# Optimization experiments

Hardware: AMD Instinct MI355X
Metric: run time of the kernel (lower is better)

Reference implementation:

```python
import jax, jax.numpy as jnp
import numpy as np

N, E, G = 32768, 262144, 512
IN_DIM, HID, HEADS = 300, 128, 4
D_FUSED = HID * HEADS  # 512
L = 3


def setup_inputs() -> dict:
    key = jax.random.key(0)
    ks = jax.random.split(key, 24)
    s = 0.02
    inp = {
        "x": jax.random.normal(ks[0], (N, IN_DIM), jnp.float32),
        "edge_index": jax.random.randint(ks[1], (2, E), 0, N, jnp.int32),
        "batch": jnp.sort(jax.random.randint(ks[2], (N,), 0, G, jnp.int32)),
        "syn_w": jax.random.normal(ks[3], (IN_DIM, HID)) * s,
        "syn_b": jnp.zeros((HID,), jnp.float32),
        "ant_w": jax.random.normal(ks[4], (IN_DIM, HID)) * s,
        "ant_b": jnp.zeros((HID,), jnp.float32),
        "fusion_w": jax.random.normal(ks[5], (2 * HID, D_FUSED)) * s,
        "fusion_b": jnp.zeros((D_FUSED,), jnp.float32),
        "Wq": jax.random.normal(ks[6], (L, D_FUSED, D_FUSED)) * s,
        "bq": jnp.zeros((L, D_FUSED), jnp.float32),
        "Wk": jax.random.normal(ks[7], (L, D_FUSED, D_FUSED)) * s,
        "bk": jnp.zeros((L, D_FUSED), jnp.float32),
        "Wv": jax.random.normal(ks[8], (L, D_FUSED, D_FUSED)) * s,
        "bv": jnp.zeros((L, D_FUSED), jnp.float32),
        "Wskip": jax.random.normal(ks[9], (L, D_FUSED, D_FUSED)) * s,
        "bskip": jnp.zeros((L, D_FUSED), jnp.float32),
        "cls_w1": jax.random.normal(ks[10], (D_FUSED, HID)) * s,
        "cls_b1": jnp.zeros((HID,), jnp.float32),
        "cls_w2": jax.random.normal(ks[11], (HID, 1)) * s,
        "cls_b2": jnp.zeros((1,), jnp.float32),
    }
    return inp


def _transformer_conv(h, src, dst, Wq, bq, Wk, bk, Wv, bv, Wskip, bskip):
    # PyG TransformerConv: per-edge dot-product attention, softmax over in-neighbors of dst,
    # concat heads, plus root/skip linear (root_weight=True, concat=True, no edge_attr).
    n = h.shape[0]
    q = (h @ Wq + bq).reshape(n, HEADS, HID)
    k = (h @ Wk + bk).reshape(n, HEADS, HID)
    v = (h @ Wv + bv).reshape(n, HEADS, HID)
    scale = 1.0 / np.sqrt(HID)
    logits = jnp.einsum("ehd,ehd->eh", q[dst], k[src]) * scale  # [E, H]
    m = jax.ops.segment_max(logits, dst, num_segments=n)        # [N, H]
    e = jnp.exp(logits - m[dst])
    z = jax.ops.segment_sum(e, dst, num_segments=n)
    alpha = e / (z[dst] + 1e-16)                                # [E, H]
    msg = alpha[:, :, None] * v[src]                            # [E, H, D]
    out = jax.ops.segment_sum(msg, dst, num_segments=n).reshape(n, D_FUSED)
    return out + h @ Wskip + bskip


def reference(x, edge_index, batch, syn_w, syn_b, ant_w, ant_b, fusion_w, fusion_b,
              Wq, bq, Wk, bk, Wv, bv, Wskip, bskip, cls_w1, cls_b1, cls_w2, cls_b2):
    x_syn = jax.nn.relu(x @ syn_w + syn_b)
    x_ant = jax.nn.relu(x @ ant_w + ant_b)
    h = jnp.concatenate([x_syn, x_ant], axis=1) @ fusion_w + fusion_b  # [N, 512]
    src, dst = edge_index[0], edge_index[1]
    for l in range(L):
        h = jax.nn.relu(_transformer_conv(h, src, dst, Wq[l], bq[l], Wk[l], bk[l],
                                          Wv[l], bv[l], Wskip[l], bskip[l]))
    cnt = jax.ops.segment_sum(jnp.ones((h.shape[0],), h.dtype), batch, num_segments=G)
    pooled = jax.ops.segment_sum(h, batch, num_segments=G) / jnp.maximum(cnt, 1.0)[:, None]
    hid = jax.nn.relu(pooled @ cls_w1 + cls_b1)
    out = jax.nn.sigmoid(hid @ cls_w2 + cls_b2)
    return out.squeeze()
```

## Files before the change

kernel.cpp:

```cpp
#include <hip/hip_runtime.h>
#include <hip/hip_bf16.h>
#include <hip/hip_fp8.h>
#include <math.h>

#define N_NODES 32768
#define N_EDGES 262144
#define N_GRAPHS 512
#define IN_DIM 300
#define KPAD 320
#define HID 128
#define HEADS 4
#define D_FUSED 512
#define N_LAYERS 3

typedef __hip_bfloat16 bf16;
typedef short bf16x8 __attribute__((ext_vector_type(8)));
typedef float f32x4 __attribute__((ext_vector_type(4)));
typedef float f32x2 __attribute__((ext_vector_type(2)));

__device__ __forceinline__ float bfs_to_f(short s)
{
    unsigned u = ((unsigned)(unsigned short)s) << 16;
    return __builtin_bit_cast(float, u);
}

__device__ __forceinline__ short f_to_bfs(float v)
{
    return (short)__builtin_bit_cast(unsigned short, __float2bfloat16(v));
}

__device__ __forceinline__ void bf8_to_f32(bf16x8 v, float* f)
{
#pragma unroll
    for (int j = 0; j < 8; ++j) f[j] = bfs_to_f(v[j]);
}

__device__ __forceinline__ unsigned char f32_to_fp8(float v)
{
#if __has_builtin(__builtin_amdgcn_cvt_pk_fp8_f32)
    int p = __builtin_amdgcn_cvt_pk_fp8_f32(v, v, 0, false);
    return (unsigned char)(p & 0xff);
#else
    __hip_fp8_e4m3 t(v);
    return (unsigned char)t.__x;
#endif
}

__device__ __forceinline__ void fp8x8_to_f32(uint2 w, float* f)
{
#if __has_builtin(__builtin_amdgcn_cvt_pk_f32_fp8)
    f32x2 a = __builtin_amdgcn_cvt_pk_f32_fp8((int)w.x, false);
    f32x2 b = __builtin_amdgcn_cvt_pk_f32_fp8((int)w.x, true);
    f32x2 c = __builtin_amdgcn_cvt_pk_f32_fp8((int)w.y, false);
    f32x2 d = __builtin_amdgcn_cvt_pk_f32_fp8((int)w.y, true);
    f[0] = a.x; f[1] = a.y; f[2] = b.x; f[3] = b.y;
    f[4] = c.x; f[5] = c.y; f[6] = d.x; f[7] = d.y;
#else
    const unsigned char* p = (const unsigned char*)&w;
#pragma unroll
    for (int j = 0; j < 8; ++j) {
        __hip_fp8_e4m3 t;
        t.__x = (__hip_fp8_storage_t)p[j];
        f[j] = (float)t;
    }
#endif
}

__device__ __forceinline__ void gload_lds16(const void* g, void* l)
{
    __builtin_amdgcn_global_load_lds(
        (const __attribute__((address_space(1))) void*)g,
        (__attribute__((address_space(3))) void*)l, 16, 0, 0);
}

template <int K, int ACT, int EPI>
__global__ __launch_bounds__(512, 2) void mfma_gemm256(
    const bf16* __restrict__ A, int lda,
    const bf16* __restrict__ Bt,
    const float* __restrict__ bias,
    bf16* __restrict__ C0, int ldc0,
    bf16* __restrict__ C1, int ldc1, int csplit,
    unsigned char* __restrict__ C2,
    int nbx)
{
    __shared__ __align__(16) char lds[131072];

    const int t = threadIdx.x;
    const int wid = t >> 6, lane = t & 63;
    const int hi = lane >> 4, li = lane & 15;
    const int wr = wid >> 2, wc = wid & 3;

    int wg = blockIdx.x;
    if ((gridDim.x & 7) == 0) {
        const int cpx = gridDim.x >> 3;
        wg = (wg & 7) * cpx + (wg >> 3);
    }
    const int mb = wg / nbx, nb = wg % nbx;
    const int brow = mb * 256, bcol = nb * 256;
    constexpr int NT = K >> 6;

    const int row0 = t >> 3, sl0 = (((t & 7) ^ (row0 & 7)) * 8);
    const int c1i = t + 512;
    const int row1 = c1i >> 3, sl1 = (((c1i & 7) ^ (row1 & 7)) * 8);

    const bf16* srcs[4][2];
    srcs[0][0] = A  + (size_t)(brow + row0)       * lda + sl0;
    srcs[0][1] = A  + (size_t)(brow + row1)       * lda + sl1;
    srcs[1][0] = A  + (size_t)(brow + 128 + row0) * lda + sl0;
    srcs[1][1] = A  + (size_t)(brow + 128 + row1) * lda + sl1;
    srcs[2][0] = Bt + (size_t)(bcol + row0)       * K   + sl0;
    srcs[2][1] = Bt + (size_t)(bcol + row1)       * K   + sl1;
    srcs[3][0] = Bt + (size_t)(bcol + 128 + row0) * K   + sl0;
    srcs[3][1] = Bt + (size_t)(bcol + 128 + row1) * K   + sl1;

    auto stage_part = [&](int buf, int kt1, int q) {
        const int ko = kt1 * 64;
        const int slab = buf * 65536 + (q >> 1) * 32768 + (q & 1) * 16384;
        gload_lds16(srcs[q][0] + ko, lds + slab + wid * 1024);
        gload_lds16(srcs[q][1] + ko, lds + slab + 8192 + wid * 1024);
    };

    f32x4 acc[8][4] = {};

#pragma unroll
    for (int q = 0; q < 4; ++q) stage_part(0, 0, q);

#pragma unroll
    for (int kt = 0; kt < NT; ++kt) {
        const int b = kt & 1;
        const char* Aslab = lds + b * 65536 + wr * 16384;
        const char* Bslab = lds + b * 65536 + 32768 + (wc >> 1) * 16384;
        const int bRow0 = (wc & 1) * 64;

        if (kt < NT - 1) {
            stage_part(b ^ 1, kt + 1, 0);
            asm volatile("s_waitcnt vmcnt(2)" ::: "memory");
        } else {
            asm volatile("s_waitcnt vmcnt(0)" ::: "memory");
        }
        __builtin_amdgcn_s_barrier();
        __builtin_amdgcn_sched_barrier(0);

        bf16x8 bfrag[4][2];
#pragma unroll
        for (int q = 0; q < 4; ++q) {
            if (q > 0 && kt < NT - 1) stage_part(b ^ 1, kt + 1, q);
            if (q == 0) {
#pragma unroll
                for (int n = 0; n < 4; ++n)
#pragma unroll
                    for (int ks = 0; ks < 2; ++ks) {
                        const int row = bRow0 + n * 16 + li;
                        bfrag[n][ks] = *(const bf16x8*)(
                            Bslab + row * 128 + (((ks * 4 + hi) ^ (row & 7)) << 4));
                    }
            }
            bf16x8 af[2][2];
#pragma unroll
            for (int mm = 0; mm < 2; ++mm)
#pragma unroll
                for (int ks = 0; ks < 2; ++ks) {
                    const int row = (q * 2 + mm) * 16 + li;
                    af[mm][ks] = *(const bf16x8*)(
                        Aslab + row * 128 + (((ks * 4 + hi) ^ (row & 7)) << 4));
                }
            __builtin_amdgcn_s_barrier();
            __builtin_amdgcn_s_setprio(1);
#pragma unroll
            for (int ks = 0; ks < 2; ++ks)
#pragma unroll
                for (int mm = 0; mm < 2; ++mm)
#pragma unroll
                    for (int n = 0; n < 4; ++n)
                        acc[q * 2 + mm][n] = __builtin_amdgcn_mfma_f32_16x16x32_bf16(
                            af[mm][ks], bfrag[n][ks], acc[q * 2 + mm][n], 0, 0, 0);
            __builtin_amdgcn_s_setprio(0);
            __builtin_amdgcn_s_barrier();
        }
    }

    if (EPI == 0) {
        const bool lo = (bcol < csplit);
        bf16* Cd = lo ? C0 : C1;
        const int ldc = lo ? ldc0 : ldc1;
        const int csub = lo ? 0 : csplit;
#pragma unroll
        for (int m = 0; m < 8; ++m)
#pragma unroll
            for (int n = 0; n < 4; ++n) {
                const int col = bcol + wc * 64 + n * 16 + li;
                const float bv = bias[col];
#pragma unroll
                for (int r = 0; r < 4; ++r) {
                    const int row = brow + wr * 128 + m * 16 + hi * 4 + r;
                    float v = acc[m][n][r] + bv;
                    if (ACT == 1) v = fmaxf(v, 0.f);
                    Cd[(size_t)row * ldc + (col - csub)] = __float2bfloat16(v);
                }
            }
    } else if (bcol < 512) {
#pragma unroll
        for (int m = 0; m < 8; ++m)
#pragma unroll
            for (int n = 0; n < 4; ++n) {
                const int col = bcol + wc * 64 + n * 16 + li;
                const float bv = bias[col];
#pragma unroll
                for (int r = 0; r < 4; ++r) {
                    const int row = brow + wr * 128 + m * 16 + hi * 4 + r;
                    C0[(size_t)row * ldc0 + col] = __float2bfloat16(acc[m][n][r] + bv);
                }
            }
    } else if (bcol < 1024) {
#pragma unroll
        for (int m = 0; m < 8; ++m)
#pragma unroll
            for (int n = 0; n < 4; ++n) {
                const int col = bcol + wc * 64 + n * 16 + li;
                const float bv = bias[col];
#pragma unroll
                for (int r = 0; r < 4; ++r) {
                    const int row = brow + wr * 128 + m * 16 + hi * 4 + r;
                    C1[(size_t)row * ldc1 + (col - 512)] = __float2bfloat16(acc[m][n][r] + bv);
                }
            }
    } else {
#pragma unroll
        for (int m = 0; m < 8; ++m)
#pragma unroll
            for (int n = 0; n < 4; ++n) {
                const int col = bcol + wc * 64 + n * 16 + li;
                const float bv = bias[col];
#pragma unroll
                for (int r = 0; r < 4; ++r) {
                    const int row = brow + wr * 128 + m * 16 + hi * 4 + r;
                    C2[(size_t)row * 1024 + (col - 1024)] = f32_to_fp8(acc[m][n][r] + bv);
                }
            }
    }
}

template <int ACT>
__global__ __launch_bounds__(256) void mfma_gemm(
    const bf16* __restrict__ A, int lda,
    const bf16* __restrict__ Bt,
    const float* __restrict__ bias,
    bf16* __restrict__ C, int ldc, int K)
{
    __shared__ __align__(16) char lds[16384];
    char* As = lds;
    char* Bs = lds + 8192;

    const int t = threadIdx.x;
    const int wid = t >> 6, lane = t & 63;
    const int brow = blockIdx.x * 128;
    const int bcol = blockIdx.y * 128;
    const int wr = wid >> 1, wc = wid & 1;

    f32x4 acc[4][4] = {};

    for (int k0 = 0; k0 < K; k0 += 32) {
#pragma unroll
        for (int j = 0; j < 2; ++j) {
            const int seg = wid * 2 + j;
            const int row = seg * 16 + (lane >> 2);
            const int clin = lane & 3;
            const int clog = clin ^ ((row >> 1) & 3);
            gload_lds16(A + (size_t)(brow + row) * lda + k0 + clog * 8,
                        As + seg * 1024);
            gload_lds16(Bt + (size_t)(bcol + row) * K + k0 + clog * 8,
                        Bs + seg * 1024);
        }
        __syncthreads();

        bf16x8 af[4], bfr[4];
#pragma unroll
        for (int m = 0; m < 4; ++m) {
            const int row = wr * 64 + m * 16 + (lane & 15);
            const int cl = (lane >> 4) ^ ((row >> 1) & 3);
            af[m] = *(const bf16x8*)(As + row * 64 + cl * 16);
        }
#pragma unroll
        for (int n = 0; n < 4; ++n) {
            const int row = wc * 64 + n * 16 + (lane & 15);
            const int cl = (lane >> 4) ^ ((row >> 1) & 3);
            bfr[n] = *(const bf16x8*)(Bs + row * 64 + cl * 16);
        }
#pragma unroll
        for (int m = 0; m < 4; ++m)
#pragma unroll
            for (int n = 0; n < 4; ++n)
                acc[m][n] = __builtin_amdgcn_mfma_f32_16x16x32_bf16(
                    af[m], bfr[n], acc[m][n], 0, 0, 0);
        __syncthreads();
    }

#pragma unroll
    for (int m = 0; m < 4; ++m) {
#pragma unroll
        for (int n = 0; n < 4; ++n) {
            const int col = bcol + wc * 64 + n * 16 + (lane & 15);
            const float bv = bias[col];
#pragma unroll
            for (int r = 0; r < 4; ++r) {
                const int row = brow + wr * 64 + m * 16 + (lane >> 4) * 4 + r;
                float v = acc[m][n][r] + bv;
                if (ACT == 1) v = fmaxf(v, 0.f);
                C[(size_t)row * ldc + col] = __float2bfloat16(v);
            }
        }
    }
}

__global__ void prep_xpad_kernel(const float* __restrict__ x, bf16* __restrict__ xb)
{
    const int n = blockIdx.x, k = threadIdx.x;
    xb[(size_t)n * KPAD + k] =
        __float2bfloat16(k < IN_DIM ? x[(size_t)n * IN_DIM + k] : 0.f);
}

__global__ void prep_encw_kernel(const float* __restrict__ syn_w,
                                 const float* __restrict__ ant_w,
                                 bf16* __restrict__ wt)
{
    const int c = blockIdx.x, k = threadIdx.x;
    float v = 0.f;
    if (k < IN_DIM) v = (c < HID) ? syn_w[k * HID + c] : ant_w[k * HID + (c - HID)];
    wt[c * KPAD + k] = __float2bfloat16(v);
}

__global__ void prep_fusw_kernel(const float* __restrict__ fw, bf16* __restrict__ wt)
{
    const int c = blockIdx.x, k = threadIdx.x;
    wt[c * 256 + k] = __float2bfloat16(fw[k * D_FUSED + c]);
}

__global__ __launch_bounds__(256) void prep_combw_kernel(
    const float* __restrict__ Wskip,
    const float* __restrict__ Wq,
    const float* __restrict__ Wk,
    const float* __restrict__ Wv,
    bf16* __restrict__ wt)
{
    __shared__ float tile[32][33];
    const int blk = blockIdx.x;
    const int l = blk >> 10, rem = blk & 1023;
    const int cb = rem >> 4, kb = rem & 15;
    const int c0 = cb * 32;

    const int sel = c0 >> 9;
    const float* mat = (sel == 0) ? Wskip : (sel == 1) ? Wq : (sel == 2) ? Wk : Wv;
    const int cp0 = c0 & 511;

    const int j = threadIdx.x & 31;
    const int i0 = threadIdx.x >> 5;
#pragma unroll
    for (int s = 0; s < 4; ++s) {
        const int i = i0 + 8 * s;
        tile[i][j] = mat[((size_t)l * 512 + kb * 32 + i) * 512 + cp0 + j];
    }
    __syncthreads();
#pragma unroll
    for (int s = 0; s < 4; ++s) {
        const int jj = i0 + 8 * s;
        wt[((size_t)l * 2048 + c0 + jj) * 512 + kb * 32 + j] =
            __float2bfloat16(tile[j][jj]);
    }
}

__global__ void prep_bias_kernel(const float* __restrict__ syn_b,
                                 const float* __restrict__ ant_b,
                                 const float* __restrict__ bskip,
                                 const float* __restrict__ bq,
                                 const float* __restrict__ bk,
                                 const float* __restrict__ bv,
                                 float* __restrict__ benc,
                                 float* __restrict__ bcomb)
{
    const int i = blockIdx.x * 256 + threadIdx.x;
    if (i < 256) benc[i] = (i < HID) ? syn_b[i] : ant_b[i - HID];
    const int j = i - 256;
    if (j >= 0 && j < 6144) {
        const int l = j >> 11, c = j & 2047;
        const int sel = c >> 9, col = c & 511;
        const float* s = (sel == 0) ? bskip : (sel == 1) ? bq : (sel == 2) ? bk : bv;
        bcomb[j] = s[l * D_FUSED + col];
    }
}

__global__ void zero_int_kernel(int* __restrict__ p, int n)
{
    int i = blockIdx.x * 256 + threadIdx.x;
    if (i < n) p[i] = 0;
}

__global__ void hist_kernel(const int* __restrict__ dst, int* __restrict__ deg, int E)
{
    int e = blockIdx.x * 256 + threadIdx.x;
    if (e < E) atomicAdd(&deg[dst[e]], 1);
}

__global__ __launch_bounds__(256) void partial_sum_kernel(const int* __restrict__ deg,
                                                          int* __restrict__ part)
{
    int v = deg[blockIdx.x * 256 + threadIdx.x];
#pragma unroll
    for (int o = 32; o; o >>= 1) v += __shfl_xor(v, o);
    __shared__ int w4[4];
    if ((threadIdx.x & 63) == 0) w4[threadIdx.x >> 6] = v;
    __syncthreads();
    if (threadIdx.x == 0) part[blockIdx.x] = w4[0] + w4[1] + w4[2] + w4[3];
}

__global__ __launch_bounds__(128) void scan_part_kernel(int* __restrict__ part)
{
    __shared__ int s[128];
    const int t = threadIdx.x;
    s[t] = part[t];
    __syncthreads();
    for (int o = 1; o < 128; o <<= 1) {
        int v = (t >= o) ? s[t - o] : 0;
        __syncthreads();
        s[t] += v;
        __syncthreads();
    }
    part[t] = (t == 0) ? 0 : s[t - 1];
}

__global__ __launch_bounds__(256) void off_kernel(const int* __restrict__ deg,
                                                  const int* __restrict__ part,
                                                  int* __restrict__ off)
{
    __shared__ int s[256];
    const int b = blockIdx.x, t = threadIdx.x;
    s[t] = deg[b * 256 + t];
    __syncthreads();
    for (int o = 1; o < 256; o <<= 1) {
        int v = (t >= o) ? s[t - o] : 0;
        __syncthreads();
        s[t] += v;
        __syncthreads();
    }
    const int excl = (t == 0) ? 0 : s[t - 1];
    off[b * 256 + t] = part[b] + excl;
    if (b == 127 && t == 255) off[N_NODES] = part[127] + s[255];
}

__global__ void scatter_kernel(const int* __restrict__ src, const int* __restrict__ dst,
                               const int* __restrict__ off, int* __restrict__ cursor,
                               int* __restrict__ csr_src, int E)
{
    int e = blockIdx.x * 256 + threadIdx.x;
    if (e < E) {
        int d = dst[e];
        int pos = atomicAdd(&cursor[d], 1);
        csr_src[off[d] + pos] = src[e];
    }
}

__global__ __launch_bounds__(256) void attn_kernel(
    const bf16* __restrict__ qb, const unsigned char* __restrict__ kvb,
    bf16* __restrict__ hout, const int* __restrict__ off,
    const int* __restrict__ csr)
{
    const int n = blockIdx.x;
    const int hd = threadIdx.x >> 6;
    const int lane = threadIdx.x & 63;
    const int g = lane >> 4, sub = lane & 15;
    const float scale = 0.08838834764831845f;

    float qf[8];
    bf8_to_f32(*(const bf16x8*)(qb + (size_t)n * 512 + hd * 128 + sub * 8), qf);

    float zA = 0.f, zB = 0.f;
    float accA[8] = {}, accB[8] = {};

    const int s0 = off[n], s1 = off[n + 1];
    for (int e0 = s0; e0 < s1; e0 += 8) {
        const int ea = e0 + g;
        const int eb = e0 + 4 + g;
        const bool va = (ea < s1);
        const bool vb = (eb < s1);
        const int sa = va ? csr[ea] : 0;
        const int sb = vb ? csr[eb] : 0;
        const unsigned char* kpa = kvb + (size_t)sa * 1024 + hd * 128 + sub * 8;
        const unsigned char* kpb = kvb + (size_t)sb * 1024 + hd * 128 + sub * 8;

        const uint2 kwa = *(const uint2*)kpa;
        const uint2 kwb = *(const uint2*)kpb;
        const uint2 vwa = *(const uint2*)(kpa + 512);
        const uint2 vwb = *(const uint2*)(kpb + 512);

        float kfa[8], kfb[8];
        fp8x8_to_f32(kwa, kfa);
        fp8x8_to_f32(kwb, kfb);
        float da = 0.f, db = 0.f;
#pragma unroll
        for (int j = 0; j < 8; ++j) {
            da = fmaf(qf[j], kfa[j], da);
            db = fmaf(qf[j], kfb[j], db);
        }
        da += __shfl_xor(da, 1);  db += __shfl_xor(db, 1);
        da += __shfl_xor(da, 2);  db += __shfl_xor(db, 2);
        da += __shfl_xor(da, 4);  db += __shfl_xor(db, 4);
        da += __shfl_xor(da, 8);  db += __shfl_xor(db, 8);

        const float wa = va ? __expf(da * scale) : 0.f;
        const float wb = vb ? __expf(db * scale) : 0.f;
        zA += wa;
        zB += wb;

        float vfa[8], vfb[8];
        fp8x8_to_f32(vwa, vfa);
        fp8x8_to_f32(vwb, vfb);
#pragma unroll
        for (int j = 0; j < 8; ++j) {
            accA[j] = fmaf(wa, vfa[j], accA[j]);
            accB[j] = fmaf(wb, vfb[j], accB[j]);
        }
    }

    float zz = zA + zB;
    zz += __shfl_xor(zz, 16);
    zz += __shfl_xor(zz, 32);
    const float inv = 1.f / (zz + 1e-16f);

    float o[8];
#pragma unroll
    for (int j = 0; j < 8; ++j) {
        float a = accA[j] + accB[j];
        a += __shfl_xor(a, 16);
        a += __shfl_xor(a, 32);
        o[j] = a * inv;
    }

    if (g == 0) {
        const size_t ob = (size_t)n * D_FUSED + hd * HID + sub * 8;
        const bf16x8 sk = *(const bf16x8*)(hout + ob);
        bf16x8 res;
#pragma unroll
        for (int j = 0; j < 8; ++j)
            res[j] = f_to_bfs(fmaxf(o[j] + bfs_to_f(sk[j]), 0.f));
        *(bf16x8*)(hout + ob) = res;
    }
}

__global__ __launch_bounds__(256) void pool_kernel(const bf16* __restrict__ h,
                                                   const int* __restrict__ batch,
                                                   float* __restrict__ pooled)
{
    const int g = blockIdx.x;
    int a = 0, b = N_NODES;
    while (a < b) { int mid = (a + b) >> 1; if (batch[mid] < g) a = mid + 1; else b = mid; }
    const int start = a;
    b = N_NODES;
    while (a < b) { int mid = (a + b) >> 1; if (batch[mid] < g + 1) a = mid + 1; else b = mid; }
    const int end = a;
    const float invc = 1.f / fmaxf((float)(end - start), 1.f);

    const int t = threadIdx.x;
    float2 s = make_float2(0.f, 0.f);
    for (int nidx = start; nidx < end; ++nidx) {
        const bf16* p = h + (size_t)nidx * D_FUSED + t * 2;
        s.x += bfs_to_f(((const short*)p)[0]);
        s.y += bfs_to_f(((const short*)p)[1]);
    }
    pooled[(size_t)g * D_FUSED + t * 2]     = s.x * invc;
    pooled[(size_t)g * D_FUSED + t * 2 + 1] = s.y * invc;
}

__global__ __launch_bounds__(128) void cls_kernel(const float* __restrict__ pooled,
                                                  const float* __restrict__ w1,
                                                  const float* __restrict__ b1,
                                                  const float* __restrict__ w2,
                                                  const float* __restrict__ b2,
                                                  float* __restrict__ out)
{
    const int g = blockIdx.x;
    const int j = threadIdx.x;
    const float* p = pooled + (size_t)g * D_FUSED;
    float acc = 0.f;
    for (int i = 0; i < D_FUSED; ++i) acc += p[i] * w1[i * HID + j];
    const float hid = fmaxf(acc + b1[j], 0.f);
    float val = hid * w2[j];
#pragma unroll
    for (int o = 32; o; o >>= 1) val += __shfl_xor(val, o);
    __shared__ float ws2[2];
    if ((threadIdx.x & 63) == 0) ws2[threadIdx.x >> 6] = val;
    __syncthreads();
    if (threadIdx.x == 0) {
        const float sum = ws2[0] + ws2[1] + b2[0];
        out[g] = 1.f / (1.f + __expf(-sum));
    }
}

extern "C" void kernel_launch(void* const* d_in, const int* in_sizes, int n_in,
                              void* d_out, int out_size, void* d_ws, size_t ws_size,
                              hipStream_t stream)
{
    const float* x        = (const float*)d_in[0];
    const int*   ei       = (const int*)d_in[1];
    const int*   batch    = (const int*)d_in[2];
    const float* syn_w    = (const float*)d_in[3];
    const float* syn_b    = (const float*)d_in[4];
    const float* ant_w    = (const float*)d_in[5];
    const float* ant_b    = (const float*)d_in[6];
    const float* fusion_w = (const float*)d_in[7];
    const float* fusion_b = (const float*)d_in[8];
    const float* Wq       = (const float*)d_in[9];
    const float* bq       = (const float*)d_in[10];
    const float* Wk       = (const float*)d_in[11];
    const float* bk       = (const float*)d_in[12];
    const float* Wv       = (const float*)d_in[13];
    const float* bv       = (const float*)d_in[14];
    const float* Wskip    = (const float*)d_in[15];
    const float* bskip    = (const float*)d_in[16];
    const float* cls_w1   = (const float*)d_in[17];
    const float* cls_b1   = (const float*)d_in[18];
    const float* cls_w2   = (const float*)d_in[19];
    const float* cls_b2   = (const float*)d_in[20];

    const int* src = ei;
    const int* dst = ei + N_EDGES;

    const size_t NV = (size_t)N_NODES * D_FUSED;
    bf16* hA    = (bf16*)d_ws;
    bf16* hB    = hA + NV;
    bf16* qbuf  = hB + NV;
    unsigned char* kvbuf = (unsigned char*)(qbuf + NV);
    bf16* wenc  = (bf16*)(kvbuf + (size_t)N_NODES * 1024);
    bf16* wfus  = wenc + 256 * KPAD;
    bf16* wcomb = wfus + 512 * 256;
    float* benc = (float*)(wcomb + (size_t)3 * 2048 * 512);
    float* bcomb = benc + 256;
    float* pooled = bcomb + 6144;
    int* deg    = (int*)(pooled + (size_t)N_GRAPHS * D_FUSED);
    int* cursor = deg + N_NODES;
    int* part   = cursor + N_NODES;
    int* off    = part + 128;
    int* csr    = off + N_NODES + 1;

    bf16* xb   = qbuf;
    bf16* tenc = hB;

    zero_int_kernel<<<(2 * N_NODES + 255) / 256, 256, 0, stream>>>(deg, 2 * N_NODES);
    hist_kernel<<<N_EDGES / 256, 256, 0, stream>>>(dst, deg, N_EDGES);
    partial_sum_kernel<<<128, 256, 0, stream>>>(deg, part);
    scan_part_kernel<<<1, 128, 0, stream>>>(part);
    off_kernel<<<128, 256, 0, stream>>>(deg, part, off);
    scatter_kernel<<<N_EDGES / 256, 256, 0, stream>>>(src, dst, off, cursor, csr, N_EDGES);

    prep_xpad_kernel<<<N_NODES, KPAD, 0, stream>>>(x, xb);
    prep_encw_kernel<<<256, KPAD, 0, stream>>>(syn_w, ant_w, wenc);
    prep_fusw_kernel<<<512, 256, 0, stream>>>(fusion_w, wfus);
    prep_combw_kernel<<<3072, 256, 0, stream>>>(Wskip, Wq, Wk, Wv, wcomb);
    prep_bias_kernel<<<25, 256, 0, stream>>>(syn_b, ant_b, bskip, bq, bk, bv, benc, bcomb);

    mfma_gemm<1><<<dim3(N_NODES / 128, 2), 256, 0, stream>>>(
        xb, KPAD, wenc, benc, tenc, 256, KPAD);
    mfma_gemm256<256, 0, 0><<<256, 512, 0, stream>>>(
        tenc, 256, wfus, fusion_b, hA, D_FUSED, hA, D_FUSED, D_FUSED, nullptr, 2);

    bf16* hcur = hA;
    bf16* hnew = hB;
    for (int l = 0; l < N_LAYERS; ++l) {
        mfma_gemm256<512, 0, 1><<<1024, 512, 0, stream>>>(
            hcur, D_FUSED, wcomb + (size_t)l * 2048 * D_FUSED,
            bcomb + (size_t)l * 2048,
            hnew, D_FUSED, qbuf, D_FUSED, 512, kvbuf, 8);
        attn_kernel<<<N_NODES, 256, 0, stream>>>(qbuf, kvbuf, hnew, off, csr);
        bf16* tmp = hcur; hcur = hnew; hnew = tmp;
    }

    pool_kernel<<<N_GRAPHS, 256, 0, stream>>>(hcur, batch, pooled);
    cls_kernel<<<N_GRAPHS, 128, 0, stream>>>(pooled, cls_w1, cls_b1, cls_w2, cls_b2,
                                             (float*)d_out);
}
```

Baseline: 582.9 us.

## Store Q in fp8 alongside K/V, vectorize x padding and pooling

The GEMM epilogue now writes Q as fp8 into one interleaved 1536-byte-per-node QKV buffer instead of a separate bf16 Q buffer, and the attention kernel reads Q, K and V from that single buffer. This halves Q write and read traffic and drops one epilogue branch, at the cost of extra quantization error on Q. Separately, the x padding kernel moves from one element per thread to float4 loads with bf16x4 stores. The pooling kernel reads 8 bf16 values per thread across four node lanes and combines them with a shared-memory reduction.

Result: faster. 563.8 us (-3.3%).

```diff
diff --git a/kernel.cpp b/kernel.cpp
--- a/kernel.cpp
+++ b/kernel.cpp
@@ -15,6 +15,7 @@
 
 typedef __hip_bfloat16 bf16;
 typedef short bf16x8 __attribute__((ext_vector_type(8)));
+typedef short bf16x4 __attribute__((ext_vector_type(4)));
 typedef float f32x4 __attribute__((ext_vector_type(4)));
 typedef float f32x2 __attribute__((ext_vector_type(2)));
 
@@ -211,7 +212,7 @@
                     C0[(size_t)row * ldc0 + col] = __float2bfloat16(acc[m][n][r] + bv);
                 }
             }
-    } else if (bcol < 1024) {
+    } else {
 #pragma unroll
         for (int m = 0; m < 8; ++m)
 #pragma unroll
@@ -221,20 +222,7 @@
 #pragma unroll
                 for (int r = 0; r < 4; ++r) {
                     const int row = brow + wr * 128 + m * 16 + hi * 4 + r;
-                    C1[(size_t)row * ldc1 + (col - 512)] = __float2bfloat16(acc[m][n][r] + bv);
-                }
-            }
-    } else {
-#pragma unroll
-        for (int m = 0; m < 8; ++m)
-#pragma unroll
-            for (int n = 0; n < 4; ++n) {
-                const int col = bcol + wc * 64 + n * 16 + li;
-                const float bv = bias[col];
-#pragma unroll
-                for (int r = 0; r < 4; ++r) {
-                    const int row = brow + wr * 128 + m * 16 + hi * 4 + r;
-                    C2[(size_t)row * 1024 + (col - 1024)] = f32_to_fp8(acc[m][n][r] + bv);
+                    C2[(size_t)row * 1536 + (col - 512)] = f32_to_fp8(acc[m][n][r] + bv);
                 }
             }
     }
@@ -314,9 +302,17 @@
 
 __global__ void prep_xpad_kernel(const float* __restrict__ x, bf16* __restrict__ xb)
 {
-    const int n = blockIdx.x, k = threadIdx.x;
-    xb[(size_t)n * KPAD + k] =
-        __float2bfloat16(k < IN_DIM ? x[(size_t)n * IN_DIM + k] : 0.f);
+    const int idx = blockIdx.x * 256 + threadIdx.x;
+    const int n = idx / 80, q = idx % 80;
+    bf16x4 o;
+    if (q < 75) {
+        const float4 v = *(const float4*)(x + (size_t)n * IN_DIM + q * 4);
+        o[0] = f_to_bfs(v.x); o[1] = f_to_bfs(v.y);
+        o[2] = f_to_bfs(v.z); o[3] = f_to_bfs(v.w);
+    } else {
+        o[0] = 0; o[1] = 0; o[2] = 0; o[3] = 0;
+    }
+    *(bf16x4*)(xb + (size_t)n * KPAD + q * 4) = o;
 }
 
 __global__ void prep_encw_kernel(const float* __restrict__ syn_w,
@@ -459,9 +455,8 @@
 }
 
 __global__ __launch_bounds__(256) void attn_kernel(
-    const bf16* __restrict__ qb, const unsigned char* __restrict__ kvb,
-    bf16* __restrict__ hout, const int* __restrict__ off,
-    const int* __restrict__ csr)
+    const unsigned char* __restrict__ qkvb, bf16* __restrict__ hout,
+    const int* __restrict__ off, const int* __restrict__ csr)
 {
     const int n = blockIdx.x;
     const int hd = threadIdx.x >> 6;
@@ -470,7 +465,7 @@
     const float scale = 0.08838834764831845f;
 
     float qf[8];
-    bf8_to_f32(*(const bf16x8*)(qb + (size_t)n * 512 + hd * 128 + sub * 8), qf);
+    fp8x8_to_f32(*(const uint2*)(qkvb + (size_t)n * 1536 + hd * 128 + sub * 8), qf);
 
     float zA = 0.f, zB = 0.f;
     float accA[8] = {}, accB[8] = {};
@@ -483,13 +478,13 @@
         const bool vb = (eb < s1);
         const int sa = va ? csr[ea] : 0;
         const int sb = vb ? csr[eb] : 0;
-        const unsigned char* kpa = kvb + (size_t)sa * 1024 + hd * 128 + sub * 8;
-        const unsigned char* kpb = kvb + (size_t)sb * 1024 + hd * 128 + sub * 8;
-
-        const uint2 kwa = *(const uint2*)kpa;
-        const uint2 kwb = *(const uint2*)kpb;
-        const uint2 vwa = *(const uint2*)(kpa + 512);
-        const uint2 vwb = *(const uint2*)(kpb + 512);
+        const unsigned char* pa = qkvb + (size_t)sa * 1536 + hd * 128 + sub * 8;
+        const unsigned char* pb = qkvb + (size_t)sb * 1536 + hd * 128 + sub * 8;
+
+        const uint2 kwa = *(const uint2*)(pa + 512);
+        const uint2 kwb = *(const uint2*)(pb + 512);
+        const uint2 vwa = *(const uint2*)(pa + 1024);
+        const uint2 vwb = *(const uint2*)(pb + 1024);
 
         float kfa[8], kfb[8];
         fp8x8_to_f32(kwa, kfa);
@@ -558,15 +553,28 @@
     const int end = a;
     const float invc = 1.f / fmaxf((float)(end - start), 1.f);
 
-    const int t = threadIdx.x;
-    float2 s = make_float2(0.f, 0.f);
-    for (int nidx = start; nidx < end; ++nidx) {
-        const bf16* p = h + (size_t)nidx * D_FUSED + t * 2;
-        s.x += bfs_to_f(((const short*)p)[0]);
-        s.y += bfs_to_f(((const short*)p)[1]);
-    }
-    pooled[(size_t)g * D_FUSED + t * 2]     = s.x * invc;
-    pooled[(size_t)g * D_FUSED + t * 2 + 1] = s.y * invc;
+    const int nl = threadIdx.x >> 6;
+    const int dl = threadIdx.x & 63;
+
+    float s[8] = {};
+    for (int nidx = start + nl; nidx < end; nidx += 4) {
+        const bf16x8 v = *(const bf16x8*)(h + (size_t)nidx * D_FUSED + dl * 8);
+#pragma unroll
+        for (int j = 0; j < 8; ++j) s[j] += bfs_to_f(v[j]);
+    }
+
+    __shared__ float red[4][512];
+#pragma unroll
+    for (int j = 0; j < 8; ++j) red[nl][dl * 8 + j] = s[j];
+    __syncthreads();
+    if (nl == 0) {
+#pragma unroll
+        for (int j = 0; j < 8; ++j) {
+            const int d = dl * 8 + j;
+            pooled[(size_t)g * D_FUSED + d] =
+                (red[0][d] + red[1][d] + red[2][d] + red[3][d]) * invc;
+        }
+    }
 }
 
 __global__ __launch_bounds__(128) void cls_kernel(const float* __restrict__ pooled,
@@ -626,9 +634,8 @@
     const size_t NV = (size_t)N_NODES * D_FUSED;
     bf16* hA    = (bf16*)d_ws;
     bf16* hB    = hA + NV;
-    bf16* qbuf  = hB + NV;
-    unsigned char* kvbuf = (unsigned char*)(qbuf + NV);
-    bf16* wenc  = (bf16*)(kvbuf + (size_t)N_NODES * 1024);
+    unsigned char* qkv = (unsigned char*)(hB + NV);
+    bf16* wenc  = (bf16*)(qkv + (size_t)N_NODES * 1536);
     bf16* wfus  = wenc + 256 * KPAD;
     bf16* wcomb = wfus + 512 * 256;
     float* benc = (float*)(wcomb + (size_t)3 * 2048 * 512);
@@ -640,7 +647,7 @@
     int* off    = part + 128;
     int* csr    = off + N_NODES + 1;
 
-    bf16* xb   = qbuf;
+    bf16* xb   = (bf16*)qkv;
     bf16* tenc = hB;
 
     zero_int_kernel<<<(2 * N_NODES + 255) / 256, 256, 0, stream>>>(deg, 2 * N_NODES);
@@ -650,7 +657,7 @@
     off_kernel<<<128, 256, 0, stream>>>(deg, part, off);
     scatter_kernel<<<N_EDGES / 256, 256, 0, stream>>>(src, dst, off, cursor, csr, N_EDGES);
 
-    prep_xpad_kernel<<<N_NODES, KPAD, 0, stream>>>(x, xb);
+    prep_xpad_kernel<<<(N_NODES * 80) / 256, 256, 0, stream>>>(x, xb);
     prep_encw_kernel<<<256, KPAD, 0, stream>>>(syn_w, ant_w, wenc);
     prep_fusw_kernel<<<512, 256, 0, stream>>>(fusion_w, wfus);
     prep_combw_kernel<<<3072, 256, 0, stream>>>(Wskip, Wq, Wk, Wv, wcomb);
@@ -667,8 +674,8 @@
         mfma_gemm256<512, 0, 1><<<1024, 512, 0, stream>>>(
             hcur, D_FUSED, wcomb + (size_t)l * 2048 * D_FUSED,
             bcomb + (size_t)l * 2048,
-            hnew, D_FUSED, qbuf, D_FUSED, 512, kvbuf, 8);
-        attn_kernel<<<N_NODES, 256, 0, stream>>>(qbuf, kvbuf, hnew, off, csr);
+            hnew, D_FUSED, nullptr, 0, 512, qkv, 8);
+        attn_kernel<<<N_NODES, 256, 0, stream>>>(qkv, hnew, off, csr);
         bf16* tmp = hcur; hcur = hnew; hnew = tmp;
     }
 
```
